# Kernel tuning notes

Hardware: AMD Instinct MI355X
Metric: run time of the kernel (lower is better)

The kernel has to match this reference:

```python
import jax, jax.numpy as jnp
import numpy as np
from jax.ops import segment_sum, segment_max

B, L, D, H, DK, NL, V, FF = 8, 256, 256, 8, 32, 4, 2048, 1024
N = B * L
EPS = 1e-5


def _ln(x, g, b):
    m = jnp.mean(x, -1, keepdims=True)
    v = jnp.var(x, -1, keepdims=True)
    return (x - m) * jax.lax.rsqrt(v + EPS) * g + b


def setup_inputs() -> dict:
    key = jax.random.key(0)
    ks = list(jax.random.split(key, 16))
    # causal decoder-decoder edges, sorted by destination (DGL 'dd' eids)
    dst_seq = np.repeat(np.arange(L), np.arange(L) + 1)
    src_seq = np.concatenate([np.arange(j + 1) for j in range(L)])
    src = jnp.asarray(np.concatenate([src_seq + b * L for b in range(B)]), jnp.int32)
    dst = jnp.asarray(np.concatenate([dst_seq + b * L for b in range(B)]), jnp.int32)
    tokens = jax.random.randint(ks[0], (N,), 0, V)
    positions = jnp.tile(jnp.arange(L), B)  # tgt[1]
    s = 0.02
    nrm = lambda k, sh: jax.random.normal(k, sh, jnp.float32) * s
    return {
        'tokens': tokens, 'positions': positions, 'src': src, 'dst': dst,
        'value_tab': nrm(ks[1], (V, D)),
        'coord_tab': nrm(ks[2], (3, D)),
        'pos_tab': nrm(ks[3], (L, D)),
        'ln1_g': jnp.ones((NL, D), jnp.float32), 'ln1_b': jnp.zeros((NL, D), jnp.float32),
        'Wq': nrm(ks[4], (NL, D, D)), 'Wk': nrm(ks[5], (NL, D, D)),
        'Wv': nrm(ks[6], (NL, D, D)), 'Wo': nrm(ks[7], (NL, D, D)),
        'ln2_g': jnp.ones((NL, D), jnp.float32), 'ln2_b': jnp.zeros((NL, D), jnp.float32),
        'W1': nrm(ks[8], (NL, D, FF)), 'b1': jnp.zeros((NL, FF), jnp.float32),
        'W2': nrm(ks[9], (NL, FF, D)), 'b2': jnp.zeros((NL, D), jnp.float32),
        'lnf_g': jnp.ones((D,), jnp.float32), 'lnf_b': jnp.zeros((D,), jnp.float32),
        'Wgen': nrm(ks[10], (D, V)), 'bgen': jnp.zeros((V,), jnp.float32),
    }


def reference(tokens, positions, src, dst, value_tab, coord_tab, pos_tab,
              ln1_g, ln1_b, Wq, Wk, Wv, Wo, ln2_g, ln2_b,
              W1, b1, W2, b2, lnf_g, lnf_b, Wgen, bgen):
    # embeddings: value*sqrt(d) + coord(pos%3) + pos(pos//3)
    x = value_tab[tokens] * jnp.sqrt(jnp.float32(D)) \
        + coord_tab[positions % 3] + pos_tab[positions // 3]
    inv_sqrt_dk = 1.0 / jnp.sqrt(jnp.float32(DK))
    for i in range(NL):
        # pre_func: layernorm + qkv projection, split heads
        xn = _ln(x, ln1_g[i], ln1_b[i])
        q = (xn @ Wq[i]).reshape(N, H, DK)
        k = (xn @ Wk[i]).reshape(N, H, DK)
        v = (xn @ Wv[i]).reshape(N, H, DK)
        # apply_edges(u_dot_v): per-edge, per-head score
        score = jnp.einsum('ehd,ehd->eh', k[src], q[dst]) * inv_sqrt_dk  # [E,H]
        # edge_softmax over edges grouped by destination node
        m = jax.lax.stop_gradient(
            segment_max(score, dst, num_segments=N, indices_are_sorted=True))
        a = jnp.exp(score - m[dst])
        denom = segment_sum(a, dst, num_segments=N, indices_are_sorted=True)
        alpha = a / denom[dst]  # [E,H]
        # send_and_recv(u_mul_e -> sum): softmax-weighted aggregation
        z = segment_sum(v[src] * alpha[..., None], dst,
                        num_segments=N, indices_are_sorted=True).reshape(N, D)
        # post_func: output proj + residual, then FFN sublayer
        x = x + z @ Wo[i]
        xn2 = _ln(x, ln2_g[i], ln2_b[i])
        x = x + (jax.nn.relu(xn2 @ W1[i] + b1[i]) @ W2[i] + b2[i])
    x = _ln(x, lnf_g, lnf_b)
    return jax.nn.log_softmax(x @ Wgen + bgen, axis=-1)  # generator
```

## Files before the change

### kernel.cpp

```cpp
#include <hip/hip_runtime.h>
#include <hip/hip_bf16.h>
#include <math.h>

constexpr int B_ = 8, L_ = 256, D_ = 256, H_ = 8, DK_ = 32, NL_ = 4, V_ = 2048, FF_ = 1024;
constexpr int N_ = B_ * L_;
constexpr float EPS_ = 1e-5f;

typedef short bf16x8 __attribute__((ext_vector_type(8)));
typedef float f32x4 __attribute__((ext_vector_type(4)));
typedef _Float16 f16x4 __attribute__((ext_vector_type(4)));

__device__ __forceinline__ short f2b(float f) {
    union { __hip_bfloat16 h; short s; } u;
    u.h = __float2bfloat16(f);
    return u.s;
}

__global__ void embed_kernel(const int* __restrict__ tokens, const int* __restrict__ positions,
                             const float* __restrict__ vtab, const float* __restrict__ ctab,
                             const float* __restrict__ ptab, float* __restrict__ x) {
    int n = blockIdx.x, d = threadIdx.x;
    int tok = tokens[n], p = positions[n];
    x[n * D_ + d] = vtab[tok * D_ + d] * 16.0f + ctab[(p % 3) * D_ + d] + ptab[(p / 3) * D_ + d];
}

__global__ void ln_kernel(const float* __restrict__ x, const float* __restrict__ g,
                          const float* __restrict__ b, short* __restrict__ out) {
    __shared__ float r1[4], r2[4], mv[2];
    int n = blockIdx.x, t = threadIdx.x;
    float v = x[n * D_ + t];
    float s1 = v, s2 = v * v;
#pragma unroll
    for (int off = 32; off; off >>= 1) {
        s1 += __shfl_down(s1, off, 64);
        s2 += __shfl_down(s2, off, 64);
    }
    int w = t >> 6;
    if ((t & 63) == 0) { r1[w] = s1; r2[w] = s2; }
    __syncthreads();
    if (t == 0) {
        float a = r1[0] + r1[1] + r1[2] + r1[3];
        float c = r2[0] + r2[1] + r2[2] + r2[3];
        float mean = a * (1.0f / D_);
        float var = c * (1.0f / D_) - mean * mean;
        mv[0] = mean;
        mv[1] = rsqrtf(var + EPS_);
    }
    __syncthreads();
    out[n * D_ + t] = f2b((v - mv[0]) * mv[1] * g[t] + b[t]);
}

__global__ void transpose_w(const float* __restrict__ src, short* __restrict__ dst, int K, int Nn) {
    __shared__ float tile[32][33];
    int n0 = blockIdx.x * 32, k0 = blockIdx.y * 32;
    size_t base = (size_t)blockIdx.z * K * Nn;
    src += base;
    dst += base;
    int tx = threadIdx.x, ty = threadIdx.y;
#pragma unroll
    for (int i = 0; i < 32; i += 8)
        tile[ty + i][tx] = src[(size_t)(k0 + ty + i) * Nn + n0 + tx];
    __syncthreads();
#pragma unroll
    for (int i = 0; i < 32; i += 8)
        dst[(size_t)(n0 + ty + i) * K + k0 + tx] = f2b(tile[tx][ty + i]);
}

template <int EPI, bool HAS_BIAS>
__device__ __forceinline__ void gemm_body(const short* __restrict__ A, const short* __restrict__ Bt,
                                          const float* __restrict__ bias, float* __restrict__ Cf,
                                          short* __restrict__ Cb, int M, int K, int Nout,
                                          int kbeg, int kend, int kz) {
    __shared__ short As[64][48];
    __shared__ short Bs[64][48];
    int t = threadIdx.x;
    int m0 = blockIdx.x * 64, n0 = blockIdx.y * 64;
    int sr = t >> 2, sc = (t & 3) * 8;
    int lane = t & 63, w = t >> 6;
    int mo = (w & 1) * 32, no = (w >> 1) * 32;
    int quad = lane >> 4, r = lane & 15;
    f32x4 acc00 = {}, acc01 = {}, acc10 = {}, acc11 = {};
    const short* Ap = &A[(size_t)(m0 + sr) * K + sc];
    const short* Bp = &Bt[(size_t)(n0 + sr) * K + sc];
    for (int k0 = kbeg; k0 < kend; k0 += 32) {
        int4 av = *(const int4*)(Ap + k0);
        int4 bv = *(const int4*)(Bp + k0);
        __syncthreads();
        *(int4*)&As[sr][sc] = av;
        *(int4*)&Bs[sr][sc] = bv;
        __syncthreads();
        bf16x8 a0 = *(const bf16x8*)&As[mo + r][quad * 8];
        bf16x8 a1 = *(const bf16x8*)&As[mo + 16 + r][quad * 8];
        bf16x8 b0 = *(const bf16x8*)&Bs[no + r][quad * 8];
        bf16x8 b1 = *(const bf16x8*)&Bs[no + 16 + r][quad * 8];
        acc00 = __builtin_amdgcn_mfma_f32_16x16x32_bf16(a0, b0, acc00, 0, 0, 0);
        acc01 = __builtin_amdgcn_mfma_f32_16x16x32_bf16(a0, b1, acc01, 0, 0, 0);
        acc10 = __builtin_amdgcn_mfma_f32_16x16x32_bf16(a1, b0, acc10, 0, 0, 0);
        acc11 = __builtin_amdgcn_mfma_f32_16x16x32_bf16(a1, b1, acc11, 0, 0, 0);
    }
#pragma unroll
    for (int i = 0; i < 2; ++i) {
#pragma unroll
        for (int j = 0; j < 2; ++j) {
            f32x4 acc = (i == 0) ? (j == 0 ? acc00 : acc01) : (j == 0 ? acc10 : acc11);
            int col = n0 + no + j * 16 + r;
            float bval = HAS_BIAS ? bias[col] : 0.f;
#pragma unroll
            for (int p = 0; p < 4; ++p) {
                int row = m0 + mo + i * 16 + quad * 4 + p;
                float v = acc[p];
                if (EPI == 0) {
                    Cf[(size_t)row * Nout + col] = v;
                } else if (EPI == 1) {
                    Cb[(size_t)row * Nout + col] = f2b(fmaxf(v + bval, 0.f));
                } else if (EPI == 2) {
                    float add = v + ((HAS_BIAS && kz == 0) ? bval : 0.f);
                    atomicAdd(&Cf[(size_t)row * Nout + col], add);
                } else if (EPI == 3) {
                    Cf[(size_t)row * Nout + col] = v + bval;
                } else if (EPI == 4) {
                    Cb[(size_t)row * Nout + col] = f2b(v);
                } else {
                    ((_Float16*)Cb)[(size_t)row * Nout + col] = (_Float16)v;
                }
            }
        }
    }
}

__global__ __launch_bounds__(256) void gemm_qkv(const short* __restrict__ A, const short* __restrict__ wq,
                                                const short* __restrict__ wk, const short* __restrict__ wv,
                                                short* __restrict__ q, short* __restrict__ k,
                                                short* __restrict__ v, int M, int K, int Nout) {
    if (blockIdx.z == 0)
        gemm_body<4, false>(A, wq, nullptr, nullptr, q, M, K, Nout, 0, K, 0);
    else if (blockIdx.z == 1)
        gemm_body<4, false>(A, wk, nullptr, nullptr, k, M, K, Nout, 0, K, 0);
    else
        gemm_body<5, false>(A, wv, nullptr, nullptr, v, M, K, Nout, 0, K, 0);
}

template <int SPLITK, bool HAS_BIAS>
__global__ __launch_bounds__(256) void gemm_accum(const short* __restrict__ A, const short* __restrict__ Bt,
                                                  const float* __restrict__ bias, float* __restrict__ C,
                                                  int M, int K, int Nout) {
    int Kp = K / SPLITK;
    int kz = blockIdx.z;
    gemm_body<2, HAS_BIAS>(A, Bt, bias, C, nullptr, M, K, Nout, kz * Kp, kz * Kp + Kp, kz);
}

__global__ __launch_bounds__(256) void gemm_biasrelu_bf16(const short* __restrict__ A,
                                                          const short* __restrict__ Bt,
                                                          const float* __restrict__ bias,
                                                          short* __restrict__ C, int M, int K, int Nout) {
    gemm_body<1, true>(A, Bt, bias, nullptr, C, M, K, Nout, 0, K, 0);
}

__global__ __launch_bounds__(256) void gemm_bias(const short* __restrict__ A, const short* __restrict__ Bt,
                                                 const float* __restrict__ bias, float* __restrict__ C,
                                                 int M, int K, int Nout) {
    gemm_body<3, true>(A, Bt, bias, C, nullptr, M, K, Nout, 0, K, 0);
}

__global__ __launch_bounds__(64) void attn_kernel(const short* __restrict__ q,
                                                  const short* __restrict__ k,
                                                  const _Float16* __restrict__ v,
                                                  short* __restrict__ z) {
    int blk = blockIdx.x;
    int bh = blk & 63;
    int qt = 15 - (blk >> 6);
    int b = bh >> 3, h = bh & 7;
    int lane = threadIdx.x;
    int r = lane & 15, quad = lane >> 4;
    int row0 = b * L_;

    bf16x8 qf = *(const bf16x8*)&q[(size_t)(row0 + qt * 16 + r) * D_ + h * DK_ + quad * 8];
    f32x4 O0 = {}, O1 = {};
    float mA = -1e30f, den = 0.f;
    int nk = qt + 1;

    bf16x8 kf = *(const bf16x8*)&k[(size_t)(row0 + r) * D_ + h * DK_ + quad * 8];
    f16x4 va, vb;
    {
        const _Float16* vp = v + (size_t)(row0 + quad * 4) * D_ + h * DK_;
#pragma unroll
        for (int i = 0; i < 4; ++i) {
            va[i] = vp[(size_t)i * D_ + r];
            vb[i] = vp[(size_t)i * D_ + 16 + r];
        }
    }
    for (int kt = 0; kt < nk; ++kt) {
        bf16x8 kf_n = kf;
        f16x4 va_n = va, vb_n = vb;
        if (kt + 1 < nk) {
            kf_n = *(const bf16x8*)&k[(size_t)(row0 + (kt + 1) * 16 + r) * D_ + h * DK_ + quad * 8];
            const _Float16* vp = v + (size_t)(row0 + (kt + 1) * 16 + quad * 4) * D_ + h * DK_;
#pragma unroll
            for (int i = 0; i < 4; ++i) {
                va_n[i] = vp[(size_t)i * D_ + r];
                vb_n[i] = vp[(size_t)i * D_ + 16 + r];
            }
        }
        f32x4 zero = {};
        f32x4 s = __builtin_amdgcn_mfma_f32_16x16x32_bf16(kf, qf, zero, 0, 0, 0);
#pragma unroll
        for (int i2 = 0; i2 < 4; ++i2) s[i2] *= 0.17677669529663687f;
        if (kt == qt) {
#pragma unroll
            for (int i2 = 0; i2 < 4; ++i2)
                if (quad * 4 + i2 > r) s[i2] = -1e30f;
        }
        float tmax = fmaxf(fmaxf(s[0], s[1]), fmaxf(s[2], s[3]));
        tmax = fmaxf(tmax, __shfl_xor(tmax, 16, 64));
        tmax = fmaxf(tmax, __shfl_xor(tmax, 32, 64));
        float mn = fmaxf(mA, tmax);
        float alpha = __expf(mA - mn);
        mA = mn;
        float p0 = __expf(s[0] - mn), p1 = __expf(s[1] - mn);
        float p2 = __expf(s[2] - mn), p3 = __expf(s[3] - mn);
        float ts = (p0 + p1) + (p2 + p3);
        ts += __shfl_xor(ts, 16, 64);
        ts += __shfl_xor(ts, 32, 64);
        den = den * alpha + ts;
        f16x4 pf;
        pf[0] = (_Float16)p0; pf[1] = (_Float16)p1; pf[2] = (_Float16)p2; pf[3] = (_Float16)p3;
        float al[4];
#pragma unroll
        for (int i2 = 0; i2 < 4; ++i2) al[i2] = __shfl(alpha, quad * 4 + i2, 64);
#pragma unroll
        for (int i2 = 0; i2 < 4; ++i2) { O0[i2] *= al[i2]; O1[i2] *= al[i2]; }
        O0 = __builtin_amdgcn_mfma_f32_16x16x16f16(pf, va, O0, 0, 0, 0);
        O1 = __builtin_amdgcn_mfma_f32_16x16x16f16(pf, vb, O1, 0, 0, 0);
        kf = kf_n; va = va_n; vb = vb_n;
    }
#pragma unroll
    for (int i2 = 0; i2 < 4; ++i2) {
        float inv = 1.0f / __shfl(den, quad * 4 + i2, 64);
        int rowz = row0 + qt * 16 + quad * 4 + i2;
        z[(size_t)rowz * D_ + h * DK_ + r] = f2b(O0[i2] * inv);
        z[(size_t)rowz * D_ + h * DK_ + 16 + r] = f2b(O1[i2] * inv);
    }
}

__global__ void lsm_kernel(float* __restrict__ logits) {
    __shared__ float rm[4], rs[4];
    int row = blockIdx.x, t = threadIdx.x;
    float* p = logits + (size_t)row * V_;
    float vals[8];
    float mx = -INFINITY;
#pragma unroll
    for (int i = 0; i < 8; ++i) {
        vals[i] = p[t + i * 256];
        mx = fmaxf(mx, vals[i]);
    }
#pragma unroll
    for (int off = 32; off; off >>= 1) mx = fmaxf(mx, __shfl_xor(mx, off, 64));
    int w = t >> 6;
    if ((t & 63) == 0) rm[w] = mx;
    __syncthreads();
    mx = fmaxf(fmaxf(rm[0], rm[1]), fmaxf(rm[2], rm[3]));
    float s = 0.f;
#pragma unroll
    for (int i = 0; i < 8; ++i) s += __expf(vals[i] - mx);
#pragma unroll
    for (int off = 32; off; off >>= 1) s += __shfl_xor(s, off, 64);
    if ((t & 63) == 0) rs[w] = s;
    __syncthreads();
    s = rs[0] + rs[1] + rs[2] + rs[3];
    float lse = mx + logf(s);
#pragma unroll
    for (int i = 0; i < 8; ++i) p[t + i * 256] = vals[i] - lse;
}

extern "C" void kernel_launch(void* const* d_in, const int* in_sizes, int n_in,
                              void* d_out, int out_size, void* d_ws, size_t ws_size,
                              hipStream_t stream) {
    const int* tokens = (const int*)d_in[0];
    const int* positions = (const int*)d_in[1];
    const float* vtab = (const float*)d_in[4];
    const float* ctab = (const float*)d_in[5];
    const float* ptab = (const float*)d_in[6];
    const float* ln1_g = (const float*)d_in[7];
    const float* ln1_b = (const float*)d_in[8];
    const float* Wq = (const float*)d_in[9];
    const float* Wk = (const float*)d_in[10];
    const float* Wv = (const float*)d_in[11];
    const float* Wo = (const float*)d_in[12];
    const float* ln2_g = (const float*)d_in[13];
    const float* ln2_b = (const float*)d_in[14];
    const float* W1 = (const float*)d_in[15];
    const float* b1 = (const float*)d_in[16];
    const float* W2 = (const float*)d_in[17];
    const float* b2 = (const float*)d_in[18];
    const float* lnf_g = (const float*)d_in[19];
    const float* lnf_b = (const float*)d_in[20];
    const float* Wgen = (const float*)d_in[21];
    const float* bgen = (const float*)d_in[22];

    char* p = (char*)d_ws;
    float* x = (float*)p;      p += (size_t)N_ * D_ * 4;
    short* qb = (short*)p;     p += (size_t)N_ * D_ * 4;
    short* kb = (short*)p;     p += (size_t)N_ * D_ * 4;
    short* vbh = (short*)p;    p += (size_t)N_ * D_ * 4;
    short* xnb = (short*)p;    p += (size_t)N_ * D_ * 2;
    short* zbb = (short*)p;    p += (size_t)N_ * D_ * 2;
    short* hbb = (short*)p;    p += (size_t)N_ * FF_ * 2;
    short* wqT = (short*)p;    p += (size_t)NL_ * D_ * D_ * 2;
    short* wkT = (short*)p;    p += (size_t)NL_ * D_ * D_ * 2;
    short* wvT = (short*)p;    p += (size_t)NL_ * D_ * D_ * 2;
    short* woT = (short*)p;    p += (size_t)NL_ * D_ * D_ * 2;
    short* w1T = (short*)p;    p += (size_t)NL_ * D_ * FF_ * 2;
    short* w2T = (short*)p;    p += (size_t)NL_ * FF_ * D_ * 2;
    short* wgT = (short*)p;    p += (size_t)D_ * V_ * 2;
    float* out = (float*)d_out;

    dim3 tb(32, 8);
    transpose_w<<<dim3(8, 8, NL_), tb, 0, stream>>>(Wq, wqT, D_, D_);
    transpose_w<<<dim3(8, 8, NL_), tb, 0, stream>>>(Wk, wkT, D_, D_);
    transpose_w<<<dim3(8, 8, NL_), tb, 0, stream>>>(Wv, wvT, D_, D_);
    transpose_w<<<dim3(8, 8, NL_), tb, 0, stream>>>(Wo, woT, D_, D_);
    transpose_w<<<dim3(32, 8, NL_), tb, 0, stream>>>(W1, w1T, D_, FF_);
    transpose_w<<<dim3(8, 32, NL_), tb, 0, stream>>>(W2, w2T, FF_, D_);
    transpose_w<<<dim3(64, 8, 1), tb, 0, stream>>>(Wgen, wgT, D_, V_);

    embed_kernel<<<N_, 256, 0, stream>>>(tokens, positions, vtab, ctab, ptab, x);
    dim3 gQKV(N_ / 64, D_ / 64, 3);
    dim3 gWo(N_ / 64, D_ / 64, 2);
    dim3 gW1(N_ / 64, FF_ / 64);
    dim3 gW2(N_ / 64, D_ / 64, 4);
    dim3 gGen(N_ / 64, V_ / 64);
    for (int i = 0; i < NL_; ++i) {
        ln_kernel<<<N_, 256, 0, stream>>>(x, ln1_g + i * D_, ln1_b + i * D_, xnb);
        gemm_qkv<<<gQKV, 256, 0, stream>>>(xnb, wqT + (size_t)i * D_ * D_, wkT + (size_t)i * D_ * D_,
                                           wvT + (size_t)i * D_ * D_, qb, kb, vbh, N_, D_, D_);
        attn_kernel<<<B_ * H_ * 16, 64, 0, stream>>>(qb, kb, (const _Float16*)vbh, zbb);
        gemm_accum<2, false><<<gWo, 256, 0, stream>>>(zbb, woT + (size_t)i * D_ * D_, nullptr, x, N_, D_, D_);
        ln_kernel<<<N_, 256, 0, stream>>>(x, ln2_g + i * D_, ln2_b + i * D_, xnb);
        gemm_biasrelu_bf16<<<gW1, 256, 0, stream>>>(xnb, w1T + (size_t)i * D_ * FF_, b1 + (size_t)i * FF_,
                                                    hbb, N_, D_, FF_);
        gemm_accum<4, true><<<gW2, 256, 0, stream>>>(hbb, w2T + (size_t)i * FF_ * D_, b2 + (size_t)i * D_,
                                                     x, N_, FF_, D_);
    }
    ln_kernel<<<N_, 256, 0, stream>>>(x, lnf_g, lnf_b, xnb);
    gemm_bias<<<gGen, 256, 0, stream>>>(xnb, wgT, bgen, out, N_, D_, V_);
    lsm_kernel<<<N_, 256, 0, stream>>>(out);
}
```

Measured before the change: 337.6 us.

## Add register prefetch and larger K tiles to GEMMs, raise split-K, merge transposes

The shared GEMM body now takes a templated K-tile size (64 or 128 instead of 32). It loads the next K-tile into registers while MFMAs run on the current shared-memory tile, which is meant to hide global load latency and cut barrier count per K. Split-K for the Wo and W2 GEMMs is doubled to create more blocks, at the cost of more atomic adds into x. The four square-weight transposes are merged into one launch to reduce launch overhead, while larger LDS tiles and register buffers may lower occupancy.

```diff
diff --git a/kernel.cpp b/kernel.cpp
--- a/kernel.cpp
+++ b/kernel.cpp
@@ -66,37 +66,77 @@
         dst[(size_t)(n0 + ty + i) * K + k0 + tx] = f2b(tile[tx][ty + i]);
 }
 
-template <int EPI, bool HAS_BIAS>
+__global__ void transpose_w4(const float* __restrict__ Wq, const float* __restrict__ Wk,
+                             const float* __restrict__ Wv, const float* __restrict__ Wo,
+                             short* __restrict__ wqT, short* __restrict__ wkT,
+                             short* __restrict__ wvT, short* __restrict__ woT) {
+    __shared__ float tile[32][33];
+    int z = blockIdx.z, m = z & 3, layer = z >> 2;
+    const float* src = (m == 0) ? Wq : (m == 1) ? Wk : (m == 2) ? Wv : Wo;
+    short* dst = (m == 0) ? wqT : (m == 1) ? wkT : (m == 2) ? wvT : woT;
+    src += (size_t)layer * D_ * D_;
+    dst += (size_t)layer * D_ * D_;
+    int n0 = blockIdx.x * 32, k0 = blockIdx.y * 32;
+    int tx = threadIdx.x, ty = threadIdx.y;
+#pragma unroll
+    for (int i = 0; i < 32; i += 8)
+        tile[ty + i][tx] = src[(size_t)(k0 + ty + i) * D_ + n0 + tx];
+    __syncthreads();
+#pragma unroll
+    for (int i = 0; i < 32; i += 8)
+        dst[(size_t)(n0 + ty + i) * D_ + k0 + tx] = f2b(tile[tx][ty + i]);
+}
+
+template <int EPI, bool HAS_BIAS, int BK>
 __device__ __forceinline__ void gemm_body(const short* __restrict__ A, const short* __restrict__ Bt,
                                           const float* __restrict__ bias, float* __restrict__ Cf,
                                           short* __restrict__ Cb, int M, int K, int Nout,
                                           int kbeg, int kend, int kz) {
-    __shared__ short As[64][48];
-    __shared__ short Bs[64][48];
+    constexpr int NI = BK / 32;
+    constexpr int STRIDE = BK + 8;
+    __shared__ short As[64][STRIDE];
+    __shared__ short Bs[64][STRIDE];
     int t = threadIdx.x;
     int m0 = blockIdx.x * 64, n0 = blockIdx.y * 64;
-    int sr = t >> 2, sc = (t & 3) * 8;
+    int sr = t >> 2, sc = (t & 3) * (BK / 4);
     int lane = t & 63, w = t >> 6;
     int mo = (w & 1) * 32, no = (w >> 1) * 32;
     int quad = lane >> 4, r = lane & 15;
     f32x4 acc00 = {}, acc01 = {}, acc10 = {}, acc11 = {};
     const short* Ap = &A[(size_t)(m0 + sr) * K + sc];
     const short* Bp = &Bt[(size_t)(n0 + sr) * K + sc];
-    for (int k0 = kbeg; k0 < kend; k0 += 32) {
-        int4 av = *(const int4*)(Ap + k0);
-        int4 bv = *(const int4*)(Bp + k0);
+    int4 aR[NI], bR[NI];
+#pragma unroll
+    for (int i = 0; i < NI; ++i) {
+        aR[i] = *(const int4*)(Ap + kbeg + i * 8);
+        bR[i] = *(const int4*)(Bp + kbeg + i * 8);
+    }
+    for (int k0 = kbeg; k0 < kend; k0 += BK) {
         __syncthreads();
-        *(int4*)&As[sr][sc] = av;
-        *(int4*)&Bs[sr][sc] = bv;
+#pragma unroll
+        for (int i = 0; i < NI; ++i) {
+            *(int4*)&As[sr][sc + i * 8] = aR[i];
+            *(int4*)&Bs[sr][sc + i * 8] = bR[i];
+        }
         __syncthreads();
-        bf16x8 a0 = *(const bf16x8*)&As[mo + r][quad * 8];
-        bf16x8 a1 = *(const bf16x8*)&As[mo + 16 + r][quad * 8];
-        bf16x8 b0 = *(const bf16x8*)&Bs[no + r][quad * 8];
-        bf16x8 b1 = *(const bf16x8*)&Bs[no + 16 + r][quad * 8];
-        acc00 = __builtin_amdgcn_mfma_f32_16x16x32_bf16(a0, b0, acc00, 0, 0, 0);
-        acc01 = __builtin_amdgcn_mfma_f32_16x16x32_bf16(a0, b1, acc01, 0, 0, 0);
-        acc10 = __builtin_amdgcn_mfma_f32_16x16x32_bf16(a1, b0, acc10, 0, 0, 0);
-        acc11 = __builtin_amdgcn_mfma_f32_16x16x32_bf16(a1, b1, acc11, 0, 0, 0);
+        if (k0 + BK < kend) {
+#pragma unroll
+            for (int i = 0; i < NI; ++i) {
+                aR[i] = *(const int4*)(Ap + k0 + BK + i * 8);
+                bR[i] = *(const int4*)(Bp + k0 + BK + i * 8);
+            }
+        }
+#pragma unroll
+        for (int kk = 0; kk < BK; kk += 32) {
+            bf16x8 a0 = *(const bf16x8*)&As[mo + r][kk + quad * 8];
+            bf16x8 a1 = *(const bf16x8*)&As[mo + 16 + r][kk + quad * 8];
+            bf16x8 b0 = *(const bf16x8*)&Bs[no + r][kk + quad * 8];
+            bf16x8 b1 = *(const bf16x8*)&Bs[no + 16 + r][kk + quad * 8];
+            acc00 = __builtin_amdgcn_mfma_f32_16x16x32_bf16(a0, b0, acc00, 0, 0, 0);
+            acc01 = __builtin_amdgcn_mfma_f32_16x16x32_bf16(a0, b1, acc01, 0, 0, 0);
+            acc10 = __builtin_amdgcn_mfma_f32_16x16x32_bf16(a1, b0, acc10, 0, 0, 0);
+            acc11 = __builtin_amdgcn_mfma_f32_16x16x32_bf16(a1, b1, acc11, 0, 0, 0);
+        }
     }
 #pragma unroll
     for (int i = 0; i < 2; ++i) {
@@ -133,33 +173,33 @@
                                                 short* __restrict__ q, short* __restrict__ k,
                                                 short* __restrict__ v, int M, int K, int Nout) {
     if (blockIdx.z == 0)
-        gemm_body<4, false>(A, wq, nullptr, nullptr, q, M, K, Nout, 0, K, 0);
+        gemm_body<4, false, 128>(A, wq, nullptr, nullptr, q, M, K, Nout, 0, K, 0);
     else if (blockIdx.z == 1)
-        gemm_body<4, false>(A, wk, nullptr, nullptr, k, M, K, Nout, 0, K, 0);
+        gemm_body<4, false, 128>(A, wk, nullptr, nullptr, k, M, K, Nout, 0, K, 0);
     else
-        gemm_body<5, false>(A, wv, nullptr, nullptr, v, M, K, Nout, 0, K, 0);
-}
-
-template <int SPLITK, bool HAS_BIAS>
+        gemm_body<5, false, 128>(A, wv, nullptr, nullptr, v, M, K, Nout, 0, K, 0);
+}
+
+template <int SPLITK, bool HAS_BIAS, int BK>
 __global__ __launch_bounds__(256) void gemm_accum(const short* __restrict__ A, const short* __restrict__ Bt,
                                                   const float* __restrict__ bias, float* __restrict__ C,
                                                   int M, int K, int Nout) {
     int Kp = K / SPLITK;
     int kz = blockIdx.z;
-    gemm_body<2, HAS_BIAS>(A, Bt, bias, C, nullptr, M, K, Nout, kz * Kp, kz * Kp + Kp, kz);
+    gemm_body<2, HAS_BIAS, BK>(A, Bt, bias, C, nullptr, M, K, Nout, kz * Kp, kz * Kp + Kp, kz);
 }
 
 __global__ __launch_bounds__(256) void gemm_biasrelu_bf16(const short* __restrict__ A,
                                                           const short* __restrict__ Bt,
                                                           const float* __restrict__ bias,
                                                           short* __restrict__ C, int M, int K, int Nout) {
-    gemm_body<1, true>(A, Bt, bias, nullptr, C, M, K, Nout, 0, K, 0);
+    gemm_body<1, true, 128>(A, Bt, bias, nullptr, C, M, K, Nout, 0, K, 0);
 }
 
 __global__ __launch_bounds__(256) void gemm_bias(const short* __restrict__ A, const short* __restrict__ Bt,
                                                  const float* __restrict__ bias, float* __restrict__ C,
                                                  int M, int K, int Nout) {
-    gemm_body<3, true>(A, Bt, bias, C, nullptr, M, K, Nout, 0, K, 0);
+    gemm_body<3, true, 128>(A, Bt, bias, C, nullptr, M, K, Nout, 0, K, 0);
 }
 
 __global__ __launch_bounds__(64) void attn_kernel(const short* __restrict__ q,
@@ -315,31 +355,28 @@
     float* out = (float*)d_out;
 
     dim3 tb(32, 8);
-    transpose_w<<<dim3(8, 8, NL_), tb, 0, stream>>>(Wq, wqT, D_, D_);
-    transpose_w<<<dim3(8, 8, NL_), tb, 0, stream>>>(Wk, wkT, D_, D_);
-    transpose_w<<<dim3(8, 8, NL_), tb, 0, stream>>>(Wv, wvT, D_, D_);
-    transpose_w<<<dim3(8, 8, NL_), tb, 0, stream>>>(Wo, woT, D_, D_);
+    transpose_w4<<<dim3(8, 8, 16), tb, 0, stream>>>(Wq, Wk, Wv, Wo, wqT, wkT, wvT, woT);
     transpose_w<<<dim3(32, 8, NL_), tb, 0, stream>>>(W1, w1T, D_, FF_);
     transpose_w<<<dim3(8, 32, NL_), tb, 0, stream>>>(W2, w2T, FF_, D_);
     transpose_w<<<dim3(64, 8, 1), tb, 0, stream>>>(Wgen, wgT, D_, V_);
 
     embed_kernel<<<N_, 256, 0, stream>>>(tokens, positions, vtab, ctab, ptab, x);
     dim3 gQKV(N_ / 64, D_ / 64, 3);
-    dim3 gWo(N_ / 64, D_ / 64, 2);
+    dim3 gWo(N_ / 64, D_ / 64, 4);
     dim3 gW1(N_ / 64, FF_ / 64);
-    dim3 gW2(N_ / 64, D_ / 64, 4);
+    dim3 gW2(N_ / 64, D_ / 64, 8);
     dim3 gGen(N_ / 64, V_ / 64);
     for (int i = 0; i < NL_; ++i) {
         ln_kernel<<<N_, 256, 0, stream>>>(x, ln1_g + i * D_, ln1_b + i * D_, xnb);
         gemm_qkv<<<gQKV, 256, 0, stream>>>(xnb, wqT + (size_t)i * D_ * D_, wkT + (size_t)i * D_ * D_,
                                            wvT + (size_t)i * D_ * D_, qb, kb, vbh, N_, D_, D_);
         attn_kernel<<<B_ * H_ * 16, 64, 0, stream>>>(qb, kb, (const _Float16*)vbh, zbb);
-        gemm_accum<2, false><<<gWo, 256, 0, stream>>>(zbb, woT + (size_t)i * D_ * D_, nullptr, x, N_, D_, D_);
+        gemm_accum<4, false, 64><<<gWo, 256, 0, stream>>>(zbb, woT + (size_t)i * D_ * D_, nullptr, x, N_, D_, D_);
         ln_kernel<<<N_, 256, 0, stream>>>(x, ln2_g + i * D_, ln2_b + i * D_, xnb);
         gemm_biasrelu_bf16<<<gW1, 256, 0, stream>>>(xnb, w1T + (size_t)i * D_ * FF_, b1 + (size_t)i * FF_,
                                                     hbb, N_, D_, FF_);
-        gemm_accum<4, true><<<gW2, 256, 0, stream>>>(hbb, w2T + (size_t)i * FF_ * D_, b2 + (size_t)i * D_,
-                                                     x, N_, FF_, D_);
+        gemm_accum<8, true, 128><<<gW2, 256, 0, stream>>>(hbb, w2T + (size_t)i * FF_ * D_, b2 + (size_t)i * D_,
+                                                          x, N_, FF_, D_);
     }
     ln_kernel<<<N_, 256, 0, stream>>>(x, lnf_g, lnf_b, xnb);
     gemm_bias<<<gGen, 256, 0, stream>>>(xnb, wgT, bgen, out, N_, D_, V_);
```

Measured after the change: 472.3 us. 39.9% more time.

## Fuse LayerNorm into GEMM prologues, transpose V output, prefetch tiles

Applied to the files above, without the earlier changes.

Removes the standalone LayerNorm kernels. Each GEMM that consumes a normalized input now computes per-row mean and rstd from the fp32 residual, then normalizes on the fly while staging A tiles into shared memory. The V projection writes a transposed fp16 layout so the attention kernel can load V with vector loads instead of strided scalar loads. The GEMM main loop also register-prefetches the next K tile, and the four square weight transposes merge into one launch. The cost is that every N-tile block redundantly recomputes row statistics and reads the fp32 input rather than bf16.

```diff
diff --git a/kernel.cpp b/kernel.cpp
--- a/kernel.cpp
+++ b/kernel.cpp
@@ -22,32 +22,6 @@
     int n = blockIdx.x, d = threadIdx.x;
     int tok = tokens[n], p = positions[n];
     x[n * D_ + d] = vtab[tok * D_ + d] * 16.0f + ctab[(p % 3) * D_ + d] + ptab[(p / 3) * D_ + d];
-}
-
-__global__ void ln_kernel(const float* __restrict__ x, const float* __restrict__ g,
-                          const float* __restrict__ b, short* __restrict__ out) {
-    __shared__ float r1[4], r2[4], mv[2];
-    int n = blockIdx.x, t = threadIdx.x;
-    float v = x[n * D_ + t];
-    float s1 = v, s2 = v * v;
-#pragma unroll
-    for (int off = 32; off; off >>= 1) {
-        s1 += __shfl_down(s1, off, 64);
-        s2 += __shfl_down(s2, off, 64);
-    }
-    int w = t >> 6;
-    if ((t & 63) == 0) { r1[w] = s1; r2[w] = s2; }
-    __syncthreads();
-    if (t == 0) {
-        float a = r1[0] + r1[1] + r1[2] + r1[3];
-        float c = r2[0] + r2[1] + r2[2] + r2[3];
-        float mean = a * (1.0f / D_);
-        float var = c * (1.0f / D_) - mean * mean;
-        mv[0] = mean;
-        mv[1] = rsqrtf(var + EPS_);
-    }
-    __syncthreads();
-    out[n * D_ + t] = f2b((v - mv[0]) * mv[1] * g[t] + b[t]);
 }
 
 __global__ void transpose_w(const float* __restrict__ src, short* __restrict__ dst, int K, int Nn) {
@@ -66,29 +40,111 @@
         dst[(size_t)(n0 + ty + i) * K + k0 + tx] = f2b(tile[tx][ty + i]);
 }
 
-template <int EPI, bool HAS_BIAS>
-__device__ __forceinline__ void gemm_body(const short* __restrict__ A, const short* __restrict__ Bt,
+__global__ void transpose_w4(const float* __restrict__ Wq, const float* __restrict__ Wk,
+                             const float* __restrict__ Wv, const float* __restrict__ Wo,
+                             short* __restrict__ wqT, short* __restrict__ wkT,
+                             short* __restrict__ wvT, short* __restrict__ woT) {
+    __shared__ float tile[32][33];
+    int z = blockIdx.z, m = z & 3, layer = z >> 2;
+    const float* src = (m == 0) ? Wq : (m == 1) ? Wk : (m == 2) ? Wv : Wo;
+    short* dst = (m == 0) ? wqT : (m == 1) ? wkT : (m == 2) ? wvT : woT;
+    src += (size_t)layer * D_ * D_;
+    dst += (size_t)layer * D_ * D_;
+    int n0 = blockIdx.x * 32, k0 = blockIdx.y * 32;
+    int tx = threadIdx.x, ty = threadIdx.y;
+#pragma unroll
+    for (int i = 0; i < 32; i += 8)
+        tile[ty + i][tx] = src[(size_t)(k0 + ty + i) * D_ + n0 + tx];
+    __syncthreads();
+#pragma unroll
+    for (int i = 0; i < 32; i += 8)
+        dst[(size_t)(n0 + ty + i) * D_ + k0 + tx] = f2b(tile[tx][ty + i]);
+}
+
+template <int EPI, bool HAS_BIAS, bool FUSE_LN>
+__device__ __forceinline__ void gemm_body(short (*As)[40], short (*Bs)[40], float (*stats)[2],
+                                          const float* __restrict__ Af, const short* __restrict__ A,
+                                          const short* __restrict__ Bt,
+                                          const float* __restrict__ lng, const float* __restrict__ lnb,
                                           const float* __restrict__ bias, float* __restrict__ Cf,
                                           short* __restrict__ Cb, int M, int K, int Nout,
                                           int kbeg, int kend, int kz) {
-    __shared__ short As[64][48];
-    __shared__ short Bs[64][48];
     int t = threadIdx.x;
     int m0 = blockIdx.x * 64, n0 = blockIdx.y * 64;
-    int sr = t >> 2, sc = (t & 3) * 8;
     int lane = t & 63, w = t >> 6;
     int mo = (w & 1) * 32, no = (w >> 1) * 32;
     int quad = lane >> 4, r = lane & 15;
+
+    if (FUSE_LN) {
+#pragma unroll 4
+        for (int rr = 0; rr < 16; ++rr) {
+            int row = m0 + w * 16 + rr;
+            float4 xv = *(const float4*)&Af[(size_t)row * K + lane * 4];
+            float s1 = (xv.x + xv.y) + (xv.z + xv.w);
+            float s2 = (xv.x * xv.x + xv.y * xv.y) + (xv.z * xv.z + xv.w * xv.w);
+#pragma unroll
+            for (int off = 1; off < 64; off <<= 1) {
+                s1 += __shfl_xor(s1, off, 64);
+                s2 += __shfl_xor(s2, off, 64);
+            }
+            if (lane == 0) {
+                float mean = s1 * (1.0f / 256.0f);
+                float var = s2 * (1.0f / 256.0f) - mean * mean;
+                stats[w * 16 + rr][0] = mean;
+                stats[w * 16 + rr][1] = rsqrtf(var + EPS_);
+            }
+        }
+        __syncthreads();
+    }
+
     f32x4 acc00 = {}, acc01 = {}, acc10 = {}, acc11 = {};
-    const short* Ap = &A[(size_t)(m0 + sr) * K + sc];
-    const short* Bp = &Bt[(size_t)(n0 + sr) * K + sc];
+    int sr = t >> 2, sc = (t & 3) * 8;
+    const short* Bg = &Bt[(size_t)(n0 + sr) * K + sc];
+    int4 bR = *(const int4*)(Bg + kbeg);
+    int4 aR;
+    float4 a0R, a1R, g0R, g1R, b0R, b1R;
+    if (FUSE_LN) {
+        const float* Ap = &Af[(size_t)(m0 + sr) * K + sc];
+        a0R = *(const float4*)(Ap + kbeg);
+        a1R = *(const float4*)(Ap + kbeg + 4);
+        g0R = *(const float4*)(lng + kbeg + sc);
+        g1R = *(const float4*)(lng + kbeg + sc + 4);
+        b0R = *(const float4*)(lnb + kbeg + sc);
+        b1R = *(const float4*)(lnb + kbeg + sc + 4);
+    } else {
+        aR = *(const int4*)(&A[(size_t)(m0 + sr) * K + sc] + kbeg);
+    }
     for (int k0 = kbeg; k0 < kend; k0 += 32) {
-        int4 av = *(const int4*)(Ap + k0);
-        int4 bv = *(const int4*)(Bp + k0);
         __syncthreads();
-        *(int4*)&As[sr][sc] = av;
-        *(int4*)&Bs[sr][sc] = bv;
+        if (FUSE_LN) {
+            float m_ = stats[sr][0], rs_ = stats[sr][1];
+            float av[8] = {a0R.x, a0R.y, a0R.z, a0R.w, a1R.x, a1R.y, a1R.z, a1R.w};
+            float gv[8] = {g0R.x, g0R.y, g0R.z, g0R.w, g1R.x, g1R.y, g1R.z, g1R.w};
+            float bv[8] = {b0R.x, b0R.y, b0R.z, b0R.w, b1R.x, b1R.y, b1R.z, b1R.w};
+            union { short s[8]; int4 v; } y;
+#pragma unroll
+            for (int p = 0; p < 8; ++p) y.s[p] = f2b((av[p] - m_) * rs_ * gv[p] + bv[p]);
+            *(int4*)&As[sr][sc] = y.v;
+        } else {
+            *(int4*)&As[sr][sc] = aR;
+        }
+        *(int4*)&Bs[sr][sc] = bR;
         __syncthreads();
+        if (k0 + 32 < kend) {
+            int kn = k0 + 32;
+            bR = *(const int4*)(Bg + kn);
+            if (FUSE_LN) {
+                const float* Ap = &Af[(size_t)(m0 + sr) * K + sc];
+                a0R = *(const float4*)(Ap + kn);
+                a1R = *(const float4*)(Ap + kn + 4);
+                g0R = *(const float4*)(lng + kn + sc);
+                g1R = *(const float4*)(lng + kn + sc + 4);
+                b0R = *(const float4*)(lnb + kn + sc);
+                b1R = *(const float4*)(lnb + kn + sc + 4);
+            } else {
+                aR = *(const int4*)(&A[(size_t)(m0 + sr) * K + sc] + kn);
+            }
+        }
         bf16x8 a0 = *(const bf16x8*)&As[mo + r][quad * 8];
         bf16x8 a1 = *(const bf16x8*)&As[mo + 16 + r][quad * 8];
         bf16x8 b0 = *(const bf16x8*)&Bs[no + r][quad * 8];
@@ -104,67 +160,85 @@
         for (int j = 0; j < 2; ++j) {
             f32x4 acc = (i == 0) ? (j == 0 ? acc00 : acc01) : (j == 0 ? acc10 : acc11);
             int col = n0 + no + j * 16 + r;
-            float bval = HAS_BIAS ? bias[col] : 0.f;
-#pragma unroll
-            for (int p = 0; p < 4; ++p) {
-                int row = m0 + mo + i * 16 + quad * 4 + p;
-                float v = acc[p];
-                if (EPI == 0) {
-                    Cf[(size_t)row * Nout + col] = v;
-                } else if (EPI == 1) {
-                    Cb[(size_t)row * Nout + col] = f2b(fmaxf(v + bval, 0.f));
-                } else if (EPI == 2) {
-                    float add = v + ((HAS_BIAS && kz == 0) ? bval : 0.f);
-                    atomicAdd(&Cf[(size_t)row * Nout + col], add);
-                } else if (EPI == 3) {
-                    Cf[(size_t)row * Nout + col] = v + bval;
-                } else if (EPI == 4) {
-                    Cb[(size_t)row * Nout + col] = f2b(v);
-                } else {
-                    ((_Float16*)Cb)[(size_t)row * Nout + col] = (_Float16)v;
+            int rbase = m0 + mo + i * 16 + quad * 4;
+            if (EPI == 6) {
+                f16x4 t4;
+#pragma unroll
+                for (int p = 0; p < 4; ++p) t4[p] = (_Float16)acc[p];
+                *(f16x4*)&((_Float16*)Cb)[(size_t)col * M + rbase] = t4;
+            } else {
+                float bval = HAS_BIAS ? bias[col] : 0.f;
+#pragma unroll
+                for (int p = 0; p < 4; ++p) {
+                    int row = rbase + p;
+                    float v = acc[p];
+                    if (EPI == 1) {
+                        Cb[(size_t)row * Nout + col] = f2b(fmaxf(v + bval, 0.f));
+                    } else if (EPI == 2) {
+                        float add = v + ((HAS_BIAS && kz == 0) ? bval : 0.f);
+                        atomicAdd(&Cf[(size_t)row * Nout + col], add);
+                    } else if (EPI == 3) {
+                        Cf[(size_t)row * Nout + col] = v + bval;
+                    } else if (EPI == 4) {
+                        Cb[(size_t)row * Nout + col] = f2b(v);
+                    }
                 }
             }
         }
     }
 }
 
-__global__ __launch_bounds__(256) void gemm_qkv(const short* __restrict__ A, const short* __restrict__ wq,
+__global__ __launch_bounds__(256) void gemm_qkv(const float* __restrict__ x, const short* __restrict__ wq,
                                                 const short* __restrict__ wk, const short* __restrict__ wv,
+                                                const float* __restrict__ lng, const float* __restrict__ lnb,
                                                 short* __restrict__ q, short* __restrict__ k,
-                                                short* __restrict__ v, int M, int K, int Nout) {
+                                                _Float16* __restrict__ vt, int M, int K, int Nout) {
+    __shared__ short As[64][40];
+    __shared__ short Bs[64][40];
+    __shared__ float stats[64][2];
     if (blockIdx.z == 0)
-        gemm_body<4, false>(A, wq, nullptr, nullptr, q, M, K, Nout, 0, K, 0);
+        gemm_body<4, false, true>(As, Bs, stats, x, nullptr, wq, lng, lnb, nullptr, nullptr, q, M, K, Nout, 0, K, 0);
     else if (blockIdx.z == 1)
-        gemm_body<4, false>(A, wk, nullptr, nullptr, k, M, K, Nout, 0, K, 0);
+        gemm_body<4, false, true>(As, Bs, stats, x, nullptr, wk, lng, lnb, nullptr, nullptr, k, M, K, Nout, 0, K, 0);
     else
-        gemm_body<5, false>(A, wv, nullptr, nullptr, v, M, K, Nout, 0, K, 0);
+        gemm_body<6, false, true>(As, Bs, stats, x, nullptr, wv, lng, lnb, nullptr, nullptr, (short*)vt, M, K, Nout, 0, K, 0);
 }
 
 template <int SPLITK, bool HAS_BIAS>
 __global__ __launch_bounds__(256) void gemm_accum(const short* __restrict__ A, const short* __restrict__ Bt,
                                                   const float* __restrict__ bias, float* __restrict__ C,
                                                   int M, int K, int Nout) {
+    __shared__ short As[64][40];
+    __shared__ short Bs[64][40];
     int Kp = K / SPLITK;
     int kz = blockIdx.z;
-    gemm_body<2, HAS_BIAS>(A, Bt, bias, C, nullptr, M, K, Nout, kz * Kp, kz * Kp + Kp, kz);
-}
-
-__global__ __launch_bounds__(256) void gemm_biasrelu_bf16(const short* __restrict__ A,
-                                                          const short* __restrict__ Bt,
-                                                          const float* __restrict__ bias,
-                                                          short* __restrict__ C, int M, int K, int Nout) {
-    gemm_body<1, true>(A, Bt, bias, nullptr, C, M, K, Nout, 0, K, 0);
-}
-
-__global__ __launch_bounds__(256) void gemm_bias(const short* __restrict__ A, const short* __restrict__ Bt,
-                                                 const float* __restrict__ bias, float* __restrict__ C,
-                                                 int M, int K, int Nout) {
-    gemm_body<3, true>(A, Bt, bias, C, nullptr, M, K, Nout, 0, K, 0);
+    gemm_body<2, HAS_BIAS, false>(As, Bs, nullptr, nullptr, A, Bt, nullptr, nullptr, bias, C, nullptr,
+                                  M, K, Nout, kz * Kp, kz * Kp + Kp, kz);
+}
+
+__global__ __launch_bounds__(256) void gemm_lnrelu(const float* __restrict__ x, const short* __restrict__ Bt,
+                                                   const float* __restrict__ lng, const float* __restrict__ lnb,
+                                                   const float* __restrict__ bias, short* __restrict__ C,
+                                                   int M, int K, int Nout) {
+    __shared__ short As[64][40];
+    __shared__ short Bs[64][40];
+    __shared__ float stats[64][2];
+    gemm_body<1, true, true>(As, Bs, stats, x, nullptr, Bt, lng, lnb, bias, nullptr, C, M, K, Nout, 0, K, 0);
+}
+
+__global__ __launch_bounds__(256) void gemm_lnbias(const float* __restrict__ x, const short* __restrict__ Bt,
+                                                   const float* __restrict__ lng, const float* __restrict__ lnb,
+                                                   const float* __restrict__ bias, float* __restrict__ C,
+                                                   int M, int K, int Nout) {
+    __shared__ short As[64][40];
+    __shared__ short Bs[64][40];
+    __shared__ float stats[64][2];
+    gemm_body<3, true, true>(As, Bs, stats, x, nullptr, Bt, lng, lnb, bias, C, nullptr, M, K, Nout, 0, K, 0);
 }
 
 __global__ __launch_bounds__(64) void attn_kernel(const short* __restrict__ q,
                                                   const short* __restrict__ k,
-                                                  const _Float16* __restrict__ v,
+                                                  const _Float16* __restrict__ vt,
                                                   short* __restrict__ z) {
     int blk = blockIdx.x;
     int bh = blk & 63;
@@ -179,27 +253,18 @@
     float mA = -1e30f, den = 0.f;
     int nk = qt + 1;
 
+    const _Float16* vta = vt + (size_t)(h * DK_ + r) * N_ + row0 + quad * 4;
+    const _Float16* vtb = vt + (size_t)(h * DK_ + 16 + r) * N_ + row0 + quad * 4;
     bf16x8 kf = *(const bf16x8*)&k[(size_t)(row0 + r) * D_ + h * DK_ + quad * 8];
-    f16x4 va, vb;
-    {
-        const _Float16* vp = v + (size_t)(row0 + quad * 4) * D_ + h * DK_;
-#pragma unroll
-        for (int i = 0; i < 4; ++i) {
-            va[i] = vp[(size_t)i * D_ + r];
-            vb[i] = vp[(size_t)i * D_ + 16 + r];
-        }
-    }
+    f16x4 va = *(const f16x4*)vta;
+    f16x4 vb = *(const f16x4*)vtb;
     for (int kt = 0; kt < nk; ++kt) {
         bf16x8 kf_n = kf;
         f16x4 va_n = va, vb_n = vb;
         if (kt + 1 < nk) {
             kf_n = *(const bf16x8*)&k[(size_t)(row0 + (kt + 1) * 16 + r) * D_ + h * DK_ + quad * 8];
-            const _Float16* vp = v + (size_t)(row0 + (kt + 1) * 16 + quad * 4) * D_ + h * DK_;
-#pragma unroll
-            for (int i = 0; i < 4; ++i) {
-                va_n[i] = vp[(size_t)i * D_ + r];
-                vb_n[i] = vp[(size_t)i * D_ + 16 + r];
-            }
+            va_n = *(const f16x4*)(vta + (kt + 1) * 16);
+            vb_n = *(const f16x4*)(vtb + (kt + 1) * 16);
         }
         f32x4 zero = {};
         f32x4 s = __builtin_amdgcn_mfma_f32_16x16x32_bf16(kf, qf, zero, 0, 0, 0);
@@ -299,10 +364,9 @@
 
     char* p = (char*)d_ws;
     float* x = (float*)p;      p += (size_t)N_ * D_ * 4;
-    short* qb = (short*)p;     p += (size_t)N_ * D_ * 4;
-    short* kb = (short*)p;     p += (size_t)N_ * D_ * 4;
-    short* vbh = (short*)p;    p += (size_t)N_ * D_ * 4;
-    short* xnb = (short*)p;    p += (size_t)N_ * D_ * 2;
+    short* qb = (short*)p;     p += (size_t)N_ * D_ * 2;
+    short* kb = (short*)p;     p += (size_t)N_ * D_ * 2;
+    _Float16* vt = (_Float16*)p; p += (size_t)D_ * N_ * 2;
     short* zbb = (short*)p;    p += (size_t)N_ * D_ * 2;
     short* hbb = (short*)p;    p += (size_t)N_ * FF_ * 2;
     short* wqT = (short*)p;    p += (size_t)NL_ * D_ * D_ * 2;
@@ -315,10 +379,7 @@
     float* out = (float*)d_out;
 
     dim3 tb(32, 8);
-    transpose_w<<<dim3(8, 8, NL_), tb, 0, stream>>>(Wq, wqT, D_, D_);
-    transpose_w<<<dim3(8, 8, NL_), tb, 0, stream>>>(Wk, wkT, D_, D_);
-    transpose_w<<<dim3(8, 8, NL_), tb, 0, stream>>>(Wv, wvT, D_, D_);
-    transpose_w<<<dim3(8, 8, NL_), tb, 0, stream>>>(Wo, woT, D_, D_);
+    transpose_w4<<<dim3(8, 8, 16), tb, 0, stream>>>(Wq, Wk, Wv, Wo, wqT, wkT, wvT, woT);
     transpose_w<<<dim3(32, 8, NL_), tb, 0, stream>>>(W1, w1T, D_, FF_);
     transpose_w<<<dim3(8, 32, NL_), tb, 0, stream>>>(W2, w2T, FF_, D_);
     transpose_w<<<dim3(64, 8, 1), tb, 0, stream>>>(Wgen, wgT, D_, V_);
@@ -330,18 +391,16 @@
     dim3 gW2(N_ / 64, D_ / 64, 4);
     dim3 gGen(N_ / 64, V_ / 64);
     for (int i = 0; i < NL_; ++i) {
-        ln_kernel<<<N_, 256, 0, stream>>>(x, ln1_g + i * D_, ln1_b + i * D_, xnb);
-        gemm_qkv<<<gQKV, 256, 0, stream>>>(xnb, wqT + (size_t)i * D_ * D_, wkT + (size_t)i * D_ * D_,
-                                           wvT + (size_t)i * D_ * D_, qb, kb, vbh, N_, D_, D_);
-        attn_kernel<<<B_ * H_ * 16, 64, 0, stream>>>(qb, kb, (const _Float16*)vbh, zbb);
+        gemm_qkv<<<gQKV, 256, 0, stream>>>(x, wqT + (size_t)i * D_ * D_, wkT + (size_t)i * D_ * D_,
+                                           wvT + (size_t)i * D_ * D_, ln1_g + i * D_, ln1_b + i * D_,
+                                           qb, kb, vt, N_, D_, D_);
+        attn_kernel<<<B_ * H_ * 16, 64, 0, stream>>>(qb, kb, vt, zbb);
         gemm_accum<2, false><<<gWo, 256, 0, stream>>>(zbb, woT + (size_t)i * D_ * D_, nullptr, x, N_, D_, D_);
-        ln_kernel<<<N_, 256, 0, stream>>>(x, ln2_g + i * D_, ln2_b + i * D_, xnb);
-        gemm_biasrelu_bf16<<<gW1, 256, 0, stream>>>(xnb, w1T + (size_t)i * D_ * FF_, b1 + (size_t)i * FF_,
-                                                    hbb, N_, D_, FF_);
+        gemm_lnrelu<<<gW1, 256, 0, stream>>>(x, w1T + (size_t)i * D_ * FF_, ln2_g + i * D_, ln2_b + i * D_,
+                                             b1 + (size_t)i * FF_, hbb, N_, D_, FF_);
         gemm_accum<4, true><<<gW2, 256, 0, stream>>>(hbb, w2T + (size_t)i * FF_ * D_, b2 + (size_t)i * D_,
                                                      x, N_, FF_, D_);
     }
-    ln_kernel<<<N_, 256, 0, stream>>>(x, lnf_g, lnf_b, xnb);
-    gemm_bias<<<gGen, 256, 0, stream>>>(xnb, wgT, bgen, out, N_, D_, V_);
+    gemm_lnbias<<<gGen, 256, 0, stream>>>(x, wgT, lnf_g, lnf_b, bgen, out, N_, D_, V_);
     lsm_kernel<<<N_, 256, 0, stream>>>(out);
 }
```

After: 379.9 us. +12.5%, slower.
